# Kernel optimization log

Measured on AMD Instinct MI355X. Metric: run time of the kernel, lower is better.

Reference implementation:

```python
import jax, jax.numpy as jnp
import numpy as np

S, B, CIN, COUT, H, W, K = 4, 32, 128, 256, 16, 16, 3
D = CIN * K * K  # 1152, patch feature size = in_features
PRIOR_PREC = 1.0  # isotropic prior precision (prior_prec_full = PRIOR_PREC * I_D)
LOG_PREC_LR = 1.0


def _patches(x, k):
    # x: [N, C, H, W] -> [N, C*k*k, H, W]; channel-major patch ordering (matches torch unfold)
    pad = k // 2
    return jax.lax.conv_general_dilated_patches(
        x, (k, k), (1, 1), ((pad, pad), (pad, pad)),
        dimension_numbers=('NCHW', 'OIHW', 'NCHW'))


def setup_inputs() -> dict:
    key = jax.random.key(0)
    k1, k2, k3, k4 = jax.random.split(key, 4)
    X = jax.random.normal(k1, (S, B, CIN, H, W), jnp.float32)
    u = jax.random.normal(k2, (B, COUT, H, W), jnp.float32)
    log_prec_scaled = jax.random.normal(k3, (B,), jnp.float32)
    Z = jax.random.normal(k4, (S, COUT, D), jnp.float32)  # standard normal noise for rsample
    return {"X": X, "u": u, "log_prec_scaled": log_prec_scaled, "Z": Z}


def reference(X, u, log_prec_scaled, Z):
    Xi = X[:, :B]  # [S, B, CIN, H, W]
    sqrt_prec = jnp.exp(0.5 * LOG_PREC_LR * log_prec_scaled)[:, None, None, None]  # [B,1,1,1]
    Xil = sqrt_prec * Xi                     # [S, B, CIN, H, W]
    Yil = sqrt_prec * u                      # [B, COUT, H, W]

    # conv_mm: sufficient statistics via patch extraction
    P = _patches(Xil.reshape(S * B, CIN, H, W), K).reshape(S, B, D, H * W)
    Yf = Yil.reshape(B, COUT, H * W)
    XLX = jnp.einsum('sbdp,sbep->sde', P, P)       # [S, D, D]
    XLY = jnp.einsum('sbdp,bcp->sdc', P, Yf)       # [S, D, COUT]

    # rsample_logpq_weights
    prec = XLX + PRIOR_PREC * jnp.eye(D, dtype=XLX.dtype)   # [S, D, D]
    L = jnp.linalg.cholesky(prec)                            # [S, D, D], lower
    logdet_prec = 2.0 * jnp.sum(jnp.log(jnp.diagonal(L, axis1=-2, axis2=-1)), -1)  # [S]

    mu = jax.scipy.linalg.cho_solve((L, True), XLY)          # [S, D, COUT]
    # dW: solve L^T dW = Z (multi-RHS; L is shared across COUT)
    dW = jax.scipy.linalg.solve_triangular(L, jnp.swapaxes(Z, -1, -2), lower=True, trans='T')
    Wm = jnp.swapaxes(mu + dW, -1, -2)                       # [S, COUT, D]

    # logP: unnormalized MVN log-prob of each output neuron's weights under N(0, PRIOR_PREC^-1 I)
    logP = (0.5 * COUT * D * jnp.log(jnp.asarray(PRIOR_PREC, Wm.dtype))
            - 0.5 * PRIOR_PREC * jnp.sum(Wm * Wm, (-1, -2)))          # [S]
    logQ = -0.5 * jnp.sum(Z * Z, (-1, -2)) + 0.5 * COUT * logdet_prec  # [S]
    logpq = logP - logQ
    return Wm, logpq
```

## Files before the change

### kernel.cpp

```cpp
#include <hip/hip_runtime.h>
#include <math.h>

#define NS 4
#define NB 32
#define CIN 128
#define NCOUT 256
#define HWN 256
#define ND 1152
#define NK 8192
static const size_t D2 = (size_t)ND * ND;

typedef __attribute__((ext_vector_type(8))) short bf16x8;
typedef __attribute__((ext_vector_type(4))) float f32x4;

static __device__ inline unsigned short f2bf(float x) {
  unsigned int u = __float_as_uint(x);
  unsigned int r = (u + 0x7fffu + ((u >> 16) & 1u)) >> 16;
  return (unsigned short)r;
}
static __device__ inline float bf2f(unsigned short h) {
  return __uint_as_float(((unsigned int)h) << 16);
}
static __device__ inline float rdlane(float v, int l) {
  return __int_as_float(__builtin_amdgcn_readlane(__float_as_int(v), l));
}


__global__ void k_sqrtp(const float* __restrict__ lp, float* __restrict__ sp,
                        float* __restrict__ pp) {
  int b = threadIdx.x;
  if (b < NB) sp[b] = expf(0.5f * lp[b]);
  if (b < 8) pp[b] = 0.f;
}

__global__ __launch_bounds__(128) void k_patches(const float* __restrict__ X,
                                                 const float* __restrict__ sp,
                                                 unsigned short* __restrict__ Phi,
                                                 unsigned short* __restrict__ Plo) {
  int d = blockIdx.x, s = blockIdx.y, t = threadIdx.x;
  int c = d / 9, r = d % 9, ky = r / 3, kx = r % 3;
  int p0 = t * 2;
  int yy = (p0 >> 4) + ky - 1;
  int xx0 = (p0 & 15) + kx - 1;
  bool oky = (yy >= 0 && yy < 16);
  bool ok0 = oky && (xx0 >= 0) && (xx0 < 16);
  bool ok1 = oky && (xx0 + 1 >= 0) && (xx0 + 1 < 16);
  int xo = yy * 16 + xx0;
  size_t base = ((size_t)s * ND + d) * NK + p0;
  for (int b = 0; b < NB; ++b) {
    float sb = sp[b];
    const float* xb = X + ((size_t)(s * NB + b) * CIN + c) * HWN;
    float v0 = ok0 ? xb[xo] * sb : 0.f;
    float v1 = ok1 ? xb[xo + 1] * sb : 0.f;
    unsigned short h0 = f2bf(v0), h1 = f2bf(v1);
    unsigned short l0 = f2bf(v0 - bf2f(h0)), l1 = f2bf(v1 - bf2f(h1));
    size_t idx = base + (size_t)b * HWN;
    *(unsigned int*)(Phi + idx) = (unsigned int)h0 | ((unsigned int)h1 << 16);
    *(unsigned int*)(Plo + idx) = (unsigned int)l0 | ((unsigned int)l1 << 16);
  }
}

__global__ __launch_bounds__(128) void k_ytt(const float* __restrict__ u,
                                             const float* __restrict__ sp,
                                             unsigned short* __restrict__ Yhi,
                                             unsigned short* __restrict__ Ylo) {
  int c = blockIdx.x, t = threadIdx.x;
  int p0 = t * 2;
  for (int b = 0; b < NB; ++b) {
    float sb = sp[b];
    const float* ub = u + ((size_t)b * NCOUT + c) * HWN + p0;
    float v0 = ub[0] * sb, v1 = ub[1] * sb;
    unsigned short h0 = f2bf(v0), h1 = f2bf(v1);
    unsigned short l0 = f2bf(v0 - bf2f(h0)), l1 = f2bf(v1 - bf2f(h1));
    size_t idx = (size_t)c * NK + (size_t)b * HWN + p0;
    *(unsigned int*)(Yhi + idx) = (unsigned int)h0 | ((unsigned int)h1 << 16);
    *(unsigned int*)(Ylo + idx) = (unsigned int)l0 | ((unsigned int)l1 << 16);
  }
}

__global__ __launch_bounds__(256) void k_gemm_mfma(
    const unsigned short* __restrict__ Phi, const unsigned short* __restrict__ Plo,
    const unsigned short* __restrict__ Yhi, const unsigned short* __restrict__ Ylo,
    float* __restrict__ prec, float* __restrict__ prec2,
    float* __restrict__ XLY, float* __restrict__ XLY2) {
  int jt = blockIdx.x, it = blockIdx.y;
  int s = blockIdx.z >> 1, kp = blockIdx.z & 1;
  bool isX = (jt <= it);
  if (!isX && jt < 9) return;
  int i0 = it * 128;
  int j0;
  const unsigned short *Bh, *Bl;
  if (isX) {
    j0 = jt * 128;
    Bh = Phi + ((size_t)s * ND + j0) * NK;
    Bl = Plo + ((size_t)s * ND + j0) * NK;
  } else {
    j0 = (jt - 9) * 128;
    Bh = Yhi + (size_t)j0 * NK;
    Bl = Ylo + (size_t)j0 * NK;
  }
  const unsigned short* Ah = Phi + ((size_t)s * ND + i0) * NK;
  const unsigned short* Al = Plo + ((size_t)s * ND + i0) * NK;

  __shared__ unsigned short sAh[4096], sAl[4096], sBh[4096], sBl[4096];
  int tid = threadIdx.x, wave = tid >> 6, lane = tid & 63;
  int wr = wave >> 1, wc = wave & 1;

  f32x4 zero = {0.f, 0.f, 0.f, 0.f};
  f32x4 acc[4][4];
#pragma unroll
  for (int m = 0; m < 4; ++m)
#pragma unroll
    for (int n = 0; n < 4; ++n) acc[m][n] = zero;

  const unsigned short* srcs[4] = {Ah, Al, Bh, Bl};
  unsigned short* dsts[4] = {sAh, sAl, sBh, sBl};
  int r0l = lane >> 2;
  int ke = (lane & 3) * 8;
  int arow0 = wr * 64 + (lane & 15);
  int brow0 = wc * 64 + (lane & 15);
  int koff = (lane >> 4) * 8;

  int kbeg = kp * (NK / 2), kend = kbeg + NK / 2;
  for (int k0 = kbeg; k0 < kend; k0 += 32) {
    __syncthreads();
#pragma unroll
    for (int f = 0; f < 4; ++f) {
#pragma unroll
      for (int cc = 0; cc < 2; ++cc) {
        int c = wave * 2 + cc;
        const unsigned short* g = srcs[f] + (size_t)(c * 16 + r0l) * NK + k0 + ke;
        unsigned short* l = dsts[f] + c * 512;
        __builtin_amdgcn_global_load_lds(
            (const __attribute__((address_space(1))) void*)g,
            (__attribute__((address_space(3))) void*)l, 16, 0, 0);
      }
    }
    __syncthreads();
    bf16x8 ah[4], al[4], bh[4], bl[4];
#pragma unroll
    for (int m = 0; m < 4; ++m) {
      int off = (arow0 + m * 16) * 32 + koff;
      ah[m] = *(const bf16x8*)&sAh[off];
      al[m] = *(const bf16x8*)&sAl[off];
    }
#pragma unroll
    for (int n = 0; n < 4; ++n) {
      int off = (brow0 + n * 16) * 32 + koff;
      bh[n] = *(const bf16x8*)&sBh[off];
      bl[n] = *(const bf16x8*)&sBl[off];
    }
#pragma unroll
    for (int m = 0; m < 4; ++m)
#pragma unroll
      for (int n = 0; n < 4; ++n) {
        acc[m][n] = __builtin_amdgcn_mfma_f32_16x16x32_bf16(ah[m], bh[n], acc[m][n], 0, 0, 0);
        acc[m][n] = __builtin_amdgcn_mfma_f32_16x16x32_bf16(ah[m], bl[n], acc[m][n], 0, 0, 0);
        acc[m][n] = __builtin_amdgcn_mfma_f32_16x16x32_bf16(al[m], bh[n], acc[m][n], 0, 0, 0);
      }
  }

  if (isX) {
    float* base = (kp ? prec2 : prec) + (size_t)s * D2;
#pragma unroll
    for (int m = 0; m < 4; ++m) {
      int row = i0 + wr * 64 + m * 16 + (lane >> 4) * 4;
#pragma unroll
      for (int n = 0; n < 4; ++n) {
        int col = j0 + wc * 64 + n * 16 + (lane & 15);
        float* cp = base + (size_t)row * ND + col;
#pragma unroll
        for (int r = 0; r < 4; ++r) cp[(size_t)r * ND] = acc[m][n][r];
      }
    }
  } else {
    float* base = (kp ? XLY2 : XLY) + (size_t)s * ND * NCOUT;
#pragma unroll
    for (int m = 0; m < 4; ++m) {
      int row = i0 + wr * 64 + m * 16 + (lane >> 4) * 4;
#pragma unroll
      for (int n = 0; n < 4; ++n) {
        int col = j0 + wc * 64 + n * 16 + (lane & 15);
        float* cp = base + (size_t)row * NCOUT + col;
#pragma unroll
        for (int r = 0; r < 4; ++r) cp[(size_t)r * NCOUT] = acc[m][n][r];
      }
    }
  }
}

__global__ __launch_bounds__(256, 3) void k_chol_dag(
    float* __restrict__ L, const float* __restrict__ Lp2,
    float* __restrict__ iA64, float* __restrict__ logd,
    int* __restrict__ flags) {
  int t0 = blockIdx.x, s = blockIdx.y;
  int bi = 0;
  while ((bi + 1) * (bi + 2) / 2 <= t0) ++bi;
  int bj = t0 - bi * (bi + 1) / 2;
  int ib = bi * 64, jb = bj * 64;
  float* Ls = L + (size_t)s * D2;
  const float* Ps = Lp2 + (size_t)s * D2;
  int* fc = flags + s * 324;

  __shared__ float At[64][68];
  __shared__ float Bt[64][68];
  int tid = threadIdx.x, tx = tid & 15, ty = tid >> 4;
  int lane = tid & 63, w = tid >> 6;

  float acc[4][4];
#pragma unroll
  for (int r = 0; r < 4; ++r) {
    size_t idx = (size_t)(ib + ty * 4 + r) * ND + jb + tx * 4;
    float4 v = *(const float4*)(Ls + idx);
    float4 v2 = *(const float4*)(Ps + idx);
    acc[r][0] = v.x + v2.x; acc[r][1] = v.y + v2.y;
    acc[r][2] = v.z + v2.z; acc[r][3] = v.w + v2.w;
  }
  if (bi == bj) {
#pragma unroll
    for (int r = 0; r < 4; ++r)
#pragma unroll
      for (int e = 0; e < 4; ++e)
        if (ty * 4 + r == tx * 4 + e) acc[r][e] += 1.f;
  }

  for (int k = 0; k < bj; ++k) {
    if (tid == 0) {
      while (__hip_atomic_load(&fc[bi * 18 + k], __ATOMIC_RELAXED,
                               __HIP_MEMORY_SCOPE_AGENT) == 0)
        __builtin_amdgcn_s_sleep(2);
      while (__hip_atomic_load(&fc[bj * 18 + k], __ATOMIC_RELAXED,
                               __HIP_MEMORY_SCOPE_AGENT) == 0)
        __builtin_amdgcn_s_sleep(2);
      (void)__hip_atomic_load(&fc[bj * 18 + k], __ATOMIC_ACQUIRE,
                              __HIP_MEMORY_SCOPE_AGENT);
    }
    __syncthreads();
    int kb = k * 64;
    {
      int a2 = tid >> 2, km = (tid & 3) * 4;
#pragma unroll
      for (int m = 0; m < 4; ++m) {
        float4 v = *(const float4*)(Ls + (size_t)(ib + a2) * ND + kb + km + m * 16);
        At[km + m * 16 + 0][a2] = v.x;
        At[km + m * 16 + 1][a2] = v.y;
        At[km + m * 16 + 2][a2] = v.z;
        At[km + m * 16 + 3][a2] = v.w;
        float4 u4 = *(const float4*)(Ls + (size_t)(jb + a2) * ND + kb + km + m * 16);
        Bt[km + m * 16 + 0][a2] = u4.x;
        Bt[km + m * 16 + 1][a2] = u4.y;
        Bt[km + m * 16 + 2][a2] = u4.z;
        Bt[km + m * 16 + 3][a2] = u4.w;
      }
    }
    __syncthreads();
#pragma unroll
    for (int kc = 0; kc < 64; ++kc) {
      float4 a4 = *(const float4*)&At[kc][ty * 4];
      float4 b4 = *(const float4*)&Bt[kc][tx * 4];
      float ar[4] = {a4.x, a4.y, a4.z, a4.w};
      float br[4] = {b4.x, b4.y, b4.z, b4.w};
#pragma unroll
      for (int r = 0; r < 4; ++r)
#pragma unroll
        for (int e = 0; e < 4; ++e) acc[r][e] = fmaf(-ar[r], br[e], acc[r][e]);
    }
    __syncthreads();
  }

  if (bi == bj) {
#pragma unroll
    for (int r = 0; r < 4; ++r)
#pragma unroll
      for (int e = 0; e < 4; ++e) At[ty * 4 + r][tx * 4 + e] = acc[r][e];
    {
      int rr = tid >> 2, cb2 = (tid & 3) * 16;
#pragma unroll
      for (int m = 0; m < 16; ++m) Bt[rr][cb2 + m] = (rr == cb2 + m) ? 1.f : 0.f;
    }
    __syncthreads();
    float diagv = 1.f;
    for (int p = 0; p < 8; ++p) {
      int c0 = p * 8;
      if (w == 0) {
        float pa[8], xb[8];
#pragma unroll
        for (int e = 0; e < 8; ++e) {
          pa[e] = At[lane][c0 + e];
          xb[e] = Bt[c0 + e][lane];
        }
#pragma unroll
        for (int j = 0; j < 8; ++j) {
          float dj = rdlane(pa[j], c0 + j);
          float r0 = __builtin_amdgcn_rsqf(dj);
          r0 = r0 * (1.5f - 0.5f * dj * r0 * r0);
          pa[j] *= r0;
          float xj = xb[j] * r0;
          xb[j] = xj;
          if (lane == c0 + j) diagv = dj * r0;
#pragma unroll
          for (int e = j + 1; e < 8; ++e) {
            float sv = rdlane(pa[j], c0 + e);
            pa[e] = fmaf(-pa[j], sv, pa[e]);
            xb[e] = fmaf(-sv, xj, xb[e]);
          }
        }
#pragma unroll
        for (int e = 0; e < 8; ++e) {
          At[lane][c0 + e] = pa[e];
          Bt[c0 + e][lane] = xb[e];
        }
      }
      __syncthreads();
      if (p < 7) {
        float La[8], Xp[8];
#pragma unroll
        for (int e = 0; e < 8; ++e) {
          La[e] = At[lane][c0 + e];
          Xp[e] = Bt[c0 + e][lane];
        }
        for (int c = c0 + 8 + w; c < 64; c += 4) {
          float Lc[8];
#pragma unroll
          for (int e = 0; e < 8; ++e) Lc[e] = At[c][c0 + e];
          float v = At[lane][c], vb = Bt[c][lane];
#pragma unroll
          for (int e = 0; e < 8; ++e) {
            v = fmaf(-La[e], Lc[e], v);
            vb = fmaf(-Lc[e], Xp[e], vb);
          }
          At[lane][c] = v;
          Bt[c][lane] = vb;
        }
        __syncthreads();
      }
    }
    if (w == 0) logd[s * ND + ib + lane] = logf(diagv);
    {
      float* q = iA64 + (size_t)(s * 18 + bi) * 4096;
      int rr = tid >> 2, cb2 = (tid & 3) * 16;
#pragma unroll
      for (int m = 0; m < 4; ++m)
        *(float4*)(q + rr * 64 + cb2 + m * 4) = *(const float4*)&Bt[rr][cb2 + m * 4];
    }
    __threadfence();
    __syncthreads();
    if (tid == 0)
      __hip_atomic_store(&fc[bi * 18 + bi], 1, __ATOMIC_RELEASE,
                         __HIP_MEMORY_SCOPE_AGENT);
  } else {
#pragma unroll
    for (int r = 0; r < 4; ++r)
#pragma unroll
      for (int e = 0; e < 4; ++e) At[tx * 4 + e][ty * 4 + r] = acc[r][e];
    __syncthreads();
    if (tid == 0) {
      while (__hip_atomic_load(&fc[bj * 18 + bj], __ATOMIC_RELAXED,
                               __HIP_MEMORY_SCOPE_AGENT) == 0)
        __builtin_amdgcn_s_sleep(2);
      (void)__hip_atomic_load(&fc[bj * 18 + bj], __ATOMIC_ACQUIRE,
                              __HIP_MEMORY_SCOPE_AGENT);
    }
    __syncthreads();
    {
      const float* q = iA64 + (size_t)(s * 18 + bj) * 4096;
      int a2 = tid >> 2, km = (tid & 3) * 4;
#pragma unroll
      for (int m = 0; m < 4; ++m) {
        float4 v = *(const float4*)(q + a2 * 64 + km + m * 16);
        Bt[km + m * 16 + 0][a2] = v.x;
        Bt[km + m * 16 + 1][a2] = v.y;
        Bt[km + m * 16 + 2][a2] = v.z;
        Bt[km + m * 16 + 3][a2] = v.w;
      }
    }
    __syncthreads();
    float acc2[4][4] = {};
#pragma unroll
    for (int kc = 0; kc < 64; ++kc) {
      float4 a4 = *(const float4*)&At[kc][ty * 4];
      float4 b4 = *(const float4*)&Bt[kc][tx * 4];
      float ar[4] = {a4.x, a4.y, a4.z, a4.w};
      float br[4] = {b4.x, b4.y, b4.z, b4.w};
#pragma unroll
      for (int r = 0; r < 4; ++r)
#pragma unroll
        for (int e = 0; e < 4; ++e) acc2[r][e] = fmaf(ar[r], br[e], acc2[r][e]);
    }
#pragma unroll
    for (int r = 0; r < 4; ++r) {
      float4 v = {acc2[r][0], acc2[r][1], acc2[r][2], acc2[r][3]};
      *(float4*)(Ls + (size_t)(ib + ty * 4 + r) * ND + jb + tx * 4) = v;
    }
    __threadfence();
    __syncthreads();
    if (tid == 0)
      __hip_atomic_store(&fc[bi * 18 + bj], 1, __ATOMIC_RELEASE,
                         __HIP_MEMORY_SCOPE_AGENT);
  }
}

__global__ __launch_bounds__(256) void k_invd128(const float* __restrict__ L,
                                                 const float* __restrict__ iA64,
                                                 float* __restrict__ iD) {
  int q = blockIdx.x, s = blockIdx.y;
  int tid = threadIdx.x;
  const float* Ls = L + (size_t)s * D2;
  float* out = iD + ((size_t)(s * 9 + q)) * 16384;
  int b0 = q * 128;
  __shared__ float inv0[64][68];
  __shared__ float invCt[64][68];
  __shared__ float Bt[64][68];
  __shared__ float Tl[64][68];

  {
    const float* iA0 = iA64 + (size_t)(s * 18 + 2 * q) * 4096;
    const float* iA1 = iA0 + 4096;
    int i = tid >> 2, c4 = (tid & 3) * 16;
#pragma unroll
    for (int m = 0; m < 4; ++m) {
      float4 v0 = *(const float4*)(iA0 + i * 64 + c4 + m * 4);
      *(float4*)&inv0[i][c4 + m * 4] = v0;
      float4 v1 = *(const float4*)(iA1 + i * 64 + c4 + m * 4);
      invCt[c4 + m * 4 + 0][i] = v1.x;
      invCt[c4 + m * 4 + 1][i] = v1.y;
      invCt[c4 + m * 4 + 2][i] = v1.z;
      invCt[c4 + m * 4 + 3][i] = v1.w;
    }
    const float* src = Ls + (size_t)(b0 + 64 + i) * ND + b0 + c4;
#pragma unroll
    for (int m = 0; m < 4; ++m) {
      float4 v = *(const float4*)(src + m * 4);
      Bt[c4 + m * 4 + 0][i] = v.x;
      Bt[c4 + m * 4 + 1][i] = v.y;
      Bt[c4 + m * 4 + 2][i] = v.z;
      Bt[c4 + m * 4 + 3][i] = v.w;
    }
  }
  __syncthreads();

  int tx = tid & 15, ty = tid >> 4;
  float acc[4][4] = {};
#pragma unroll
  for (int k = 0; k < 64; ++k) {
    float a4[4], b4[4];
#pragma unroll
    for (int e = 0; e < 4; ++e) { a4[e] = Bt[k][ty * 4 + e]; b4[e] = inv0[k][tx * 4 + e]; }
#pragma unroll
    for (int r = 0; r < 4; ++r)
#pragma unroll
      for (int e = 0; e < 4; ++e) acc[r][e] = fmaf(a4[r], b4[e], acc[r][e]);
  }
#pragma unroll
  for (int r = 0; r < 4; ++r)
#pragma unroll
    for (int e = 0; e < 4; ++e) Tl[ty * 4 + r][tx * 4 + e] = acc[r][e];
  __syncthreads();
  float acc2[4][4] = {};
#pragma unroll
  for (int k = 0; k < 64; ++k) {
    float a4[4], b4[4];
#pragma unroll
    for (int e = 0; e < 4; ++e) { a4[e] = invCt[k][ty * 4 + e]; b4[e] = Tl[k][tx * 4 + e]; }
#pragma unroll
    for (int r = 0; r < 4; ++r)
#pragma unroll
      for (int e = 0; e < 4; ++e) acc2[r][e] = fmaf(a4[r], b4[e], acc2[r][e]);
  }
  {
    int rrow = tid >> 2, cc = (tid & 3) * 32;
    float* o = out + rrow * 128 + cc;
    if (cc < 64) {
#pragma unroll
      for (int m = 0; m < 8; ++m) {
        float4 v = {inv0[rrow][cc + m * 4 + 0], inv0[rrow][cc + m * 4 + 1],
                    inv0[rrow][cc + m * 4 + 2], inv0[rrow][cc + m * 4 + 3]};
        *(float4*)(o + m * 4) = v;
      }
    } else {
      float4 z = {0.f, 0.f, 0.f, 0.f};
#pragma unroll
      for (int m = 0; m < 8; ++m) *(float4*)(o + m * 4) = z;
    }
  }
#pragma unroll
  for (int r = 0; r < 4; ++r) {
    float4 v = {-acc2[r][0], -acc2[r][1], -acc2[r][2], -acc2[r][3]};
    *(float4*)(out + (size_t)(64 + ty * 4 + r) * 128 + tx * 4) = v;
  }
  {
    int i = tid >> 2, jc = (tid & 3) * 16;
#pragma unroll
    for (int m = 0; m < 4; ++m) {
      float4 v = {invCt[jc + m * 4 + 0][i], invCt[jc + m * 4 + 1][i],
                  invCt[jc + m * 4 + 2][i], invCt[jc + m * 4 + 3][i]};
      *(float4*)(out + (size_t)(64 + i) * 128 + 64 + jc + m * 4) = v;
    }
  }
}

__global__ __launch_bounds__(256) void k_solve2(
    const float* __restrict__ L, const float* __restrict__ iD,
    const float* __restrict__ B1, const float* __restrict__ B2,
    const float* __restrict__ Z, float* __restrict__ Xf, float* __restrict__ Xb,
    float* __restrict__ Wm, float* __restrict__ pp, int* __restrict__ flags) {
  int r = blockIdx.x, ct = blockIdx.y, s = blockIdx.z;
  int rb = r * 128, cb = ct * 64;
  const float* Ls = L + (size_t)s * D2;
  const float* Dq = iD + ((size_t)(s * 9 + r)) * 16384;
  float* Xfs = Xf + (size_t)s * ND * NCOUT;
  float* Xbs = Xb + (size_t)s * ND * NCOUT;
  int fbf = 1296 + (s * 4 + ct) * 9;
  int fbb = 1440 + (s * 4 + ct) * 9;

  __shared__ float sA[32][132];
  __shared__ float sB[32][68];
  __shared__ float red[8];
  int tid = threadIdx.x, tx = tid & 15, ty = tid >> 4;
  int wave = tid >> 6, lane = tid & 63;

  float acc[8][4];
#pragma unroll
  for (int ii = 0; ii < 8; ++ii) {
    size_t idx = (size_t)s * ND * NCOUT + (size_t)(rb + ty * 8 + ii) * NCOUT + cb + tx * 4;
    float4 v = *(const float4*)(B1 + idx);
    float4 v2 = *(const float4*)(B2 + idx);
    acc[ii][0] = v.x + v2.x; acc[ii][1] = v.y + v2.y;
    acc[ii][2] = v.z + v2.z; acc[ii][3] = v.w + v2.w;
  }
  for (int q = 0; q < r; ++q) {
    if (tid == 0) {
      while (__hip_atomic_load(&flags[fbf + q], __ATOMIC_RELAXED,
                               __HIP_MEMORY_SCOPE_AGENT) == 0)
        __builtin_amdgcn_s_sleep(2);
      (void)__hip_atomic_load(&flags[fbf + q], __ATOMIC_ACQUIRE,
                              __HIP_MEMORY_SCOPE_AGENT);
    }
    __syncthreads();
    int qb = q * 128;
    for (int kk = 0; kk < 4; ++kk) {
      __syncthreads();
      {
        int i = tid >> 1, kb = (tid & 1) * 16;
        const float* src = Ls + (size_t)(rb + i) * ND + qb + kk * 32 + kb;
#pragma unroll
        for (int m = 0; m < 4; ++m) {
          float4 v = *(const float4*)(src + m * 4);
          sA[kb + m * 4 + 0][i] = v.x;
          sA[kb + m * 4 + 1][i] = v.y;
          sA[kb + m * 4 + 2][i] = v.z;
          sA[kb + m * 4 + 3][i] = v.w;
        }
      }
      {
        int k = tid >> 3, jb2 = (tid & 7) * 8;
        const float* src = Xfs + (size_t)(qb + kk * 32 + k) * NCOUT + cb + jb2;
        float4 v0 = *(const float4*)src;
        float4 v1 = *(const float4*)(src + 4);
        *(float4*)&sB[k][jb2] = v0;
        *(float4*)&sB[k][jb2 + 4] = v1;
      }
      __syncthreads();
#pragma unroll
      for (int k = 0; k < 32; ++k) {
        float4 a0 = *(const float4*)&sA[k][ty * 8];
        float4 a1 = *(const float4*)&sA[k][ty * 8 + 4];
        float4 b0 = *(const float4*)&sB[k][tx * 4];
        float a[8] = {a0.x, a0.y, a0.z, a0.w, a1.x, a1.y, a1.z, a1.w};
        float b[4] = {b0.x, b0.y, b0.z, b0.w};
#pragma unroll
        for (int ii = 0; ii < 8; ++ii)
#pragma unroll
          for (int j = 0; j < 4; ++j) acc[ii][j] = fmaf(-a[ii], b[j], acc[ii][j]);
      }
    }
  }
  float acc2[8][4] = {};
  for (int kk = 0; kk < 4; ++kk) {
    __syncthreads();
    if ((ty >> 2) == kk) {
      int kloc = ty * 8 - kk * 32;
#pragma unroll
      for (int ii = 0; ii < 8; ++ii) {
        float4 v = {acc[ii][0], acc[ii][1], acc[ii][2], acc[ii][3]};
        *(float4*)&sB[kloc + ii][tx * 4] = v;
      }
    }
    {
      int i = tid >> 1, kb = (tid & 1) * 16;
      const float* src = Dq + (size_t)i * 128 + kk * 32 + kb;
#pragma unroll
      for (int m = 0; m < 4; ++m) {
        float4 v = *(const float4*)(src + m * 4);
        sA[kb + m * 4 + 0][i] = v.x;
        sA[kb + m * 4 + 1][i] = v.y;
        sA[kb + m * 4 + 2][i] = v.z;
        sA[kb + m * 4 + 3][i] = v.w;
      }
    }
    __syncthreads();
#pragma unroll
    for (int k = 0; k < 32; ++k) {
      float4 a0 = *(const float4*)&sA[k][ty * 8];
      float4 a1 = *(const float4*)&sA[k][ty * 8 + 4];
      float4 b0 = *(const float4*)&sB[k][tx * 4];
      float a[8] = {a0.x, a0.y, a0.z, a0.w, a1.x, a1.y, a1.z, a1.w};
      float b[4] = {b0.x, b0.y, b0.z, b0.w};
#pragma unroll
      for (int ii = 0; ii < 8; ++ii)
#pragma unroll
        for (int j = 0; j < 4; ++j) acc2[ii][j] = fmaf(a[ii], b[j], acc2[ii][j]);
    }
  }
#pragma unroll
  for (int ii = 0; ii < 8; ++ii) {
    float4 v = {acc2[ii][0], acc2[ii][1], acc2[ii][2], acc2[ii][3]};
    *(float4*)(Xfs + (size_t)(rb + ty * 8 + ii) * NCOUT + cb + tx * 4) = v;
  }
  __threadfence();
  __syncthreads();
  if (tid == 0)
    __hip_atomic_store(&flags[fbf + r], 1, __ATOMIC_RELEASE,
                       __HIP_MEMORY_SCOPE_AGENT);

#pragma unroll
  for (int ii = 0; ii < 8; ++ii)
#pragma unroll
    for (int j = 0; j < 4; ++j) acc[ii][j] = acc2[ii][j];

  float zp = 0.f;
  for (int kk = 0; kk < 4; ++kk) {
    __syncthreads();
    {
      int c = tid >> 2, d8 = (tid & 3) * 8;
      const float* src = Z + ((size_t)(s * NCOUT) + cb + c) * ND + rb + kk * 32 + d8;
      float4 v0 = *(const float4*)src;
      float4 v1 = *(const float4*)(src + 4);
      sA[d8 + 0][c] = v0.x; sA[d8 + 1][c] = v0.y; sA[d8 + 2][c] = v0.z; sA[d8 + 3][c] = v0.w;
      sA[d8 + 4][c] = v1.x; sA[d8 + 5][c] = v1.y; sA[d8 + 6][c] = v1.z; sA[d8 + 7][c] = v1.w;
      zp += v0.x * v0.x + v0.y * v0.y + v0.z * v0.z + v0.w * v0.w;
      zp += v1.x * v1.x + v1.y * v1.y + v1.z * v1.z + v1.w * v1.w;
    }
    __syncthreads();
    if ((ty >> 2) == kk) {
      int kloc = ty * 8 - kk * 32;
#pragma unroll
      for (int ii = 0; ii < 8; ++ii) {
        float4 v = *(const float4*)&sA[kloc + ii][tx * 4];
        acc[ii][0] += v.x; acc[ii][1] += v.y; acc[ii][2] += v.z; acc[ii][3] += v.w;
      }
    }
  }
#pragma unroll
  for (int m2 = 32; m2 >= 1; m2 >>= 1) zp += __shfl_xor(zp, m2, 64);
  if (lane == 0) red[wave] = zp;
  __syncthreads();
  if (tid == 0) atomicAdd(pp + s, red[0] + red[1] + red[2] + red[3]);

  for (int q = 8; q > r; --q) {
    if (tid == 0) {
      while (__hip_atomic_load(&flags[fbb + q], __ATOMIC_RELAXED,
                               __HIP_MEMORY_SCOPE_AGENT) == 0)
        __builtin_amdgcn_s_sleep(2);
      (void)__hip_atomic_load(&flags[fbb + q], __ATOMIC_ACQUIRE,
                              __HIP_MEMORY_SCOPE_AGENT);
    }
    __syncthreads();
    int qb = q * 128;
    for (int kk = 0; kk < 4; ++kk) {
      __syncthreads();
      {
        int k = tid >> 3, ib2 = (tid & 7) * 16;
        const float* src = Ls + (size_t)(qb + kk * 32 + k) * ND + rb + ib2;
#pragma unroll
        for (int m = 0; m < 4; ++m)
          *(float4*)&sA[k][ib2 + m * 4] = *(const float4*)(src + m * 4);
      }
      {
        int k = tid >> 3, jb2 = (tid & 7) * 8;
        const float* src = Xbs + (size_t)(qb + kk * 32 + k) * NCOUT + cb + jb2;
        float4 v0 = *(const float4*)src;
        float4 v1 = *(const float4*)(src + 4);
        *(float4*)&sB[k][jb2] = v0;
        *(float4*)&sB[k][jb2 + 4] = v1;
      }
      __syncthreads();
#pragma unroll
      for (int k = 0; k < 32; ++k) {
        float4 a0 = *(const float4*)&sA[k][ty * 8];
        float4 a1 = *(const float4*)&sA[k][ty * 8 + 4];
        float4 b0 = *(const float4*)&sB[k][tx * 4];
        float a[8] = {a0.x, a0.y, a0.z, a0.w, a1.x, a1.y, a1.z, a1.w};
        float b[4] = {b0.x, b0.y, b0.z, b0.w};
#pragma unroll
        for (int ii = 0; ii < 8; ++ii)
#pragma unroll
          for (int j = 0; j < 4; ++j) acc[ii][j] = fmaf(-a[ii], b[j], acc[ii][j]);
      }
    }
  }
#pragma unroll
  for (int ii = 0; ii < 8; ++ii)
#pragma unroll
    for (int j = 0; j < 4; ++j) acc2[ii][j] = 0.f;
  for (int kk = 0; kk < 4; ++kk) {
    __syncthreads();
    if ((ty >> 2) == kk) {
      int kloc = ty * 8 - kk * 32;
#pragma unroll
      for (int ii = 0; ii < 8; ++ii) {
        float4 v = {acc[ii][0], acc[ii][1], acc[ii][2], acc[ii][3]};
        *(float4*)&sB[kloc + ii][tx * 4] = v;
      }
    }
    {
      int k = tid >> 3, ib2 = (tid & 7) * 16;
      const float* src = Dq + (size_t)(kk * 32 + k) * 128 + ib2;
#pragma unroll
      for (int m = 0; m < 4; ++m)
        *(float4*)&sA[k][ib2 + m * 4] = *(const float4*)(src + m * 4);
    }
    __syncthreads();
#pragma unroll
    for (int k = 0; k < 32; ++k) {
      float4 a0 = *(const float4*)&sA[k][ty * 8];
      float4 a1 = *(const float4*)&sA[k][ty * 8 + 4];
      float4 b0 = *(const float4*)&sB[k][tx * 4];
      float a[8] = {a0.x, a0.y, a0.z, a0.w, a1.x, a1.y, a1.z, a1.w};
      float b[4] = {b0.x, b0.y, b0.z, b0.w};
#pragma unroll
      for (int ii = 0; ii < 8; ++ii)
#pragma unroll
        for (int j = 0; j < 4; ++j) acc2[ii][j] = fmaf(a[ii], b[j], acc2[ii][j]);
    }
  }
#pragma unroll
  for (int ii = 0; ii < 8; ++ii) {
    float4 v = {acc2[ii][0], acc2[ii][1], acc2[ii][2], acc2[ii][3]};
    *(float4*)(Xbs + (size_t)(rb + ty * 8 + ii) * NCOUT + cb + tx * 4) = v;
  }
  __threadfence();
  __syncthreads();
  if (tid == 0)
    __hip_atomic_store(&flags[fbb + r], 1, __ATOMIC_RELEASE,
                       __HIP_MEMORY_SCOPE_AGENT);
  float wp = 0.f;
#pragma unroll
  for (int ii = 0; ii < 8; ++ii)
#pragma unroll
    for (int j = 0; j < 4; ++j) wp += acc2[ii][j] * acc2[ii][j];
#pragma unroll
  for (int m2 = 32; m2 >= 1; m2 >>= 1) wp += __shfl_xor(wp, m2, 64);
  __syncthreads();
  if (lane == 0) red[wave] = wp;
  __syncthreads();
  if (tid == 0) atomicAdd(pp + 4 + s, red[0] + red[1] + red[2] + red[3]);
  for (int kk = 0; kk < 4; ++kk) {
    __syncthreads();
    if ((ty >> 2) == kk) {
      int kloc = ty * 8 - kk * 32;
#pragma unroll
      for (int ii = 0; ii < 8; ++ii) {
        float4 v = {acc2[ii][0], acc2[ii][1], acc2[ii][2], acc2[ii][3]};
        *(float4*)&sB[kloc + ii][tx * 4] = v;
      }
    }
    __syncthreads();
    {
      int c = tid >> 2, d8 = (tid & 3) * 8;
      float t0 = sB[d8 + 0][c], t1 = sB[d8 + 1][c], t2 = sB[d8 + 2][c], t3 = sB[d8 + 3][c];
      float t4 = sB[d8 + 4][c], t5 = sB[d8 + 5][c], t6 = sB[d8 + 6][c], t7 = sB[d8 + 7][c];
      float* dst = Wm + ((size_t)(s * NCOUT) + cb + c) * ND + rb + kk * 32 + d8;
      float4 w0 = {t0, t1, t2, t3}, w1 = {t4, t5, t6, t7};
      *(float4*)dst = w0;
      *(float4*)(dst + 4) = w1;
    }
  }
}

__global__ __launch_bounds__(256) void k_finalize(const float* __restrict__ logd,
                                                  const float* __restrict__ pp,
                                                  float* __restrict__ out) {
  int s = blockIdx.x, tid = threadIdx.x;
  __shared__ float r0[256];
  float l = 0.f;
  for (int i = tid; i < ND; i += 256) l += logd[s * ND + i];
  r0[tid] = l;
  __syncthreads();
  for (int off = 128; off; off >>= 1) {
    if (tid < off) r0[tid] += r0[tid + off];
    __syncthreads();
  }
  if (tid == 0) {
    float logdet = 2.0f * r0[0];
    out[s] = 0.5f * (pp[s] - pp[4 + s]) - 128.0f * logdet;
  }
}

extern "C" void kernel_launch(void* const* d_in, const int* in_sizes, int n_in,
                              void* d_out, int out_size, void* d_ws, size_t ws_size,
                              hipStream_t stream) {
  const float* X = (const float*)d_in[0];
  const float* u = (const float*)d_in[1];
  const float* lp = (const float*)d_in[2];
  const float* Z = (const float*)d_in[3];
  float* out = (float*)d_out;

  float* ws = (float*)d_ws;
  float* sp    = ws;
  float* invd  = sp + 64;
  float* logd  = invd + (size_t)NS * ND;
  float* pp    = logd + (size_t)NS * ND;
  int*   flags = (int*)(pp + 64);
  float* iD    = (float*)(flags + 2048);
  float* iA64  = iD + (size_t)NS * 9 * 16384;
  float* Xf    = iA64 + (size_t)NS * 18 * 4096;
  float* Xb    = Xf + (size_t)NS * ND * NCOUT;
  float* prec  = Xb + (size_t)NS * ND * NCOUT;
  float* prec2 = prec + (size_t)NS * D2;
  float* XLY   = prec2 + (size_t)NS * D2;
  float* XLY2  = XLY + (size_t)NS * ND * NCOUT;
  unsigned short* Phi = (unsigned short*)(XLY2 + (size_t)NS * ND * NCOUT);
  unsigned short* Plo = Phi + (size_t)NS * ND * NK;
  unsigned short* Yhi = Plo + (size_t)NS * ND * NK;
  unsigned short* Ylo = Yhi + (size_t)NCOUT * NK;

  hipMemsetAsync(flags, 0, 2048 * sizeof(int), stream);
  k_sqrtp<<<1, 64, 0, stream>>>(lp, sp, pp);
  k_patches<<<dim3(ND, NS), 128, 0, stream>>>(X, sp, Phi, Plo);
  k_ytt<<<NCOUT, 128, 0, stream>>>(u, sp, Yhi, Ylo);
  k_gemm_mfma<<<dim3(11, 9, NS * 2), 256, 0, stream>>>(Phi, Plo, Yhi, Ylo, prec,
                                                       prec2, XLY, XLY2);
  k_chol_dag<<<dim3(171, NS), 256, 0, stream>>>(prec, prec2, iA64, logd, flags);
  k_invd128<<<dim3(9, NS), 256, 0, stream>>>(prec, iA64, iD);
  k_solve2<<<dim3(9, 4, NS), 256, 0, stream>>>(prec, iD, XLY, XLY2, Z, Xf, Xb,
                                               out, pp, flags);
  k_finalize<<<NS, 256, 0, stream>>>(logd, pp, out + (size_t)NS * NCOUT * ND);
}
```

Before: 1.391 ms.

## Fuse diagonal-block Cholesky into last off-diagonal panel block; spin on flags in all threads

The factorization of each diagonal 64x64 block (except the first) moves into the block that computes the last sub-diagonal panel (bj == bi-1). That block applies the final rank-64 update itself and factors immediately, instead of a separate diagonal block waiting on flags. This removes one inter-block flag hop per step on the Cholesky critical path. A new set of flags (pd) signals when the partially updated diagonal tile has been written to global memory. Flag waits are now a helper in which every thread spins with a shorter sleep, replacing the tid==0 spin plus __syncthreads. This relies on the flags buffer being large enough and zeroed for the new pd region, and adds global traffic for the staged diagonal tile.

```diff
diff --git a/kernel.cpp b/kernel.cpp
--- a/kernel.cpp
+++ b/kernel.cpp
@@ -23,6 +23,11 @@
 }
 static __device__ inline float rdlane(float v, int l) {
   return __int_as_float(__builtin_amdgcn_readlane(__float_as_int(v), l));
+}
+static __device__ __forceinline__ void waitflag(const int* f) {
+  while (__hip_atomic_load(f, __ATOMIC_RELAXED, __HIP_MEMORY_SCOPE_AGENT) == 0)
+    __builtin_amdgcn_s_sleep(1);
+  (void)__hip_atomic_load(f, __ATOMIC_ACQUIRE, __HIP_MEMORY_SCOPE_AGENT);
 }
 
 
@@ -189,6 +194,92 @@
   }
 }
 
+
+static __device__ __forceinline__ void factor64(
+    float acc[4][4], float (&At)[64][68], float (&Bt)[64][68],
+    int tid, int lane, int w, int tx, int ty,
+    float* iA64q, float* logdq, int* flagq) {
+  __syncthreads();
+#pragma unroll
+  for (int r = 0; r < 4; ++r)
+#pragma unroll
+    for (int e = 0; e < 4; ++e) At[ty * 4 + r][tx * 4 + e] = acc[r][e];
+  {
+    int rr = tid >> 2, cb2 = (tid & 3) * 16;
+#pragma unroll
+    for (int m = 0; m < 16; ++m) Bt[rr][cb2 + m] = (rr == cb2 + m) ? 1.f : 0.f;
+  }
+  __syncthreads();
+  float diagv = 1.f;
+  for (int p = 0; p < 8; ++p) {
+    int c0 = p * 8;
+    if (w == 0) {
+      float pa[8], xb[8];
+#pragma unroll
+      for (int e = 0; e < 8; ++e) {
+        pa[e] = At[lane][c0 + e];
+        xb[e] = Bt[c0 + e][lane];
+      }
+#pragma unroll
+      for (int j = 0; j < 8; ++j) {
+        float dj = rdlane(pa[j], c0 + j);
+        float r0 = __builtin_amdgcn_rsqf(dj);
+        r0 = r0 * (1.5f - 0.5f * dj * r0 * r0);
+        pa[j] *= r0;
+        float xj = xb[j] * r0;
+        xb[j] = xj;
+        if (lane == c0 + j) diagv = dj * r0;
+#pragma unroll
+        for (int e = j + 1; e < 8; ++e) {
+          float sv = rdlane(pa[j], c0 + e);
+          pa[e] = fmaf(-pa[j], sv, pa[e]);
+          xb[e] = fmaf(-sv, xj, xb[e]);
+        }
+      }
+#pragma unroll
+      for (int e = 0; e < 8; ++e) {
+        At[lane][c0 + e] = pa[e];
+        Bt[c0 + e][lane] = xb[e];
+      }
+    }
+    __syncthreads();
+    if (p < 7) {
+      float La[8], Xp[8];
+#pragma unroll
+      for (int e = 0; e < 8; ++e) {
+        La[e] = At[lane][c0 + e];
+        Xp[e] = Bt[c0 + e][lane];
+      }
+      for (int c = c0 + 8 + w; c < 64; c += 4) {
+        float Lc[8];
+#pragma unroll
+        for (int e = 0; e < 8; ++e) Lc[e] = At[c][c0 + e];
+        float v = At[lane][c], vb = Bt[c][lane];
+#pragma unroll
+        for (int e = 0; e < 8; ++e) {
+          v = fmaf(-La[e], Lc[e], v);
+          vb = fmaf(-Lc[e], Xp[e], vb);
+        }
+        At[lane][c] = v;
+        Bt[c][lane] = vb;
+      }
+      __syncthreads();
+    }
+  }
+  if (w == 0) logdq[lane] = logf(diagv);
+  {
+    float* q = iA64q;
+    int rr = tid >> 2, cb2 = (tid & 3) * 16;
+#pragma unroll
+    for (int m = 0; m < 4; ++m)
+      *(float4*)(q + rr * 64 + cb2 + m * 4) = *(const float4*)&Bt[rr][cb2 + m * 4];
+  }
+  __threadfence();
+  __syncthreads();
+  if (tid == 0)
+    __hip_atomic_store(flagq, 1, __ATOMIC_RELEASE, __HIP_MEMORY_SCOPE_AGENT);
+}
+
 __global__ __launch_bounds__(256, 3) void k_chol_dag(
     float* __restrict__ L, const float* __restrict__ Lp2,
     float* __restrict__ iA64, float* __restrict__ logd,
@@ -201,6 +292,7 @@
   float* Ls = L + (size_t)s * D2;
   const float* Ps = Lp2 + (size_t)s * D2;
   int* fc = flags + s * 324;
+  int* pd = flags + 1584 + s * 18;
 
   __shared__ float At[64][68];
   __shared__ float Bt[64][68];
@@ -225,17 +317,8 @@
   }
 
   for (int k = 0; k < bj; ++k) {
-    if (tid == 0) {
-      while (__hip_atomic_load(&fc[bi * 18 + k], __ATOMIC_RELAXED,
-                               __HIP_MEMORY_SCOPE_AGENT) == 0)
-        __builtin_amdgcn_s_sleep(2);
-      while (__hip_atomic_load(&fc[bj * 18 + k], __ATOMIC_RELAXED,
-                               __HIP_MEMORY_SCOPE_AGENT) == 0)
-        __builtin_amdgcn_s_sleep(2);
-      (void)__hip_atomic_load(&fc[bj * 18 + k], __ATOMIC_ACQUIRE,
-                              __HIP_MEMORY_SCOPE_AGENT);
-    }
-    __syncthreads();
+    waitflag(&fc[bi * 18 + k]);
+    waitflag(&fc[bj * 18 + k]);
     int kb = k * 64;
     {
       int a2 = tid >> 2, km = (tid & 3) * 4;
@@ -269,99 +352,27 @@
   }
 
   if (bi == bj) {
+    if (bi == 0) {
+      factor64(acc, At, Bt, tid, lane, w, tx, ty,
+               iA64 + (size_t)(s * 18) * 4096, logd + (size_t)s * ND, &fc[0]);
+    } else {
+#pragma unroll
+      for (int r = 0; r < 4; ++r) {
+        float4 v = {acc[r][0], acc[r][1], acc[r][2], acc[r][3]};
+        *(float4*)(Ls + (size_t)(ib + ty * 4 + r) * ND + ib + tx * 4) = v;
+      }
+      __threadfence();
+      __syncthreads();
+      if (tid == 0)
+        __hip_atomic_store(&pd[bi], 1, __ATOMIC_RELEASE,
+                           __HIP_MEMORY_SCOPE_AGENT);
+    }
+  } else {
 #pragma unroll
     for (int r = 0; r < 4; ++r)
 #pragma unroll
-      for (int e = 0; e < 4; ++e) At[ty * 4 + r][tx * 4 + e] = acc[r][e];
-    {
-      int rr = tid >> 2, cb2 = (tid & 3) * 16;
-#pragma unroll
-      for (int m = 0; m < 16; ++m) Bt[rr][cb2 + m] = (rr == cb2 + m) ? 1.f : 0.f;
-    }
-    __syncthreads();
-    float diagv = 1.f;
-    for (int p = 0; p < 8; ++p) {
-      int c0 = p * 8;
-      if (w == 0) {
-        float pa[8], xb[8];
-#pragma unroll
-        for (int e = 0; e < 8; ++e) {
-          pa[e] = At[lane][c0 + e];
-          xb[e] = Bt[c0 + e][lane];
-        }
-#pragma unroll
-        for (int j = 0; j < 8; ++j) {
-          float dj = rdlane(pa[j], c0 + j);
-          float r0 = __builtin_amdgcn_rsqf(dj);
-          r0 = r0 * (1.5f - 0.5f * dj * r0 * r0);
-          pa[j] *= r0;
-          float xj = xb[j] * r0;
-          xb[j] = xj;
-          if (lane == c0 + j) diagv = dj * r0;
-#pragma unroll
-          for (int e = j + 1; e < 8; ++e) {
-            float sv = rdlane(pa[j], c0 + e);
-            pa[e] = fmaf(-pa[j], sv, pa[e]);
-            xb[e] = fmaf(-sv, xj, xb[e]);
-          }
-        }
-#pragma unroll
-        for (int e = 0; e < 8; ++e) {
-          At[lane][c0 + e] = pa[e];
-          Bt[c0 + e][lane] = xb[e];
-        }
-      }
-      __syncthreads();
-      if (p < 7) {
-        float La[8], Xp[8];
-#pragma unroll
-        for (int e = 0; e < 8; ++e) {
-          La[e] = At[lane][c0 + e];
-          Xp[e] = Bt[c0 + e][lane];
-        }
-        for (int c = c0 + 8 + w; c < 64; c += 4) {
-          float Lc[8];
-#pragma unroll
-          for (int e = 0; e < 8; ++e) Lc[e] = At[c][c0 + e];
-          float v = At[lane][c], vb = Bt[c][lane];
-#pragma unroll
-          for (int e = 0; e < 8; ++e) {
-            v = fmaf(-La[e], Lc[e], v);
-            vb = fmaf(-Lc[e], Xp[e], vb);
-          }
-          At[lane][c] = v;
-          Bt[c][lane] = vb;
-        }
-        __syncthreads();
-      }
-    }
-    if (w == 0) logd[s * ND + ib + lane] = logf(diagv);
-    {
-      float* q = iA64 + (size_t)(s * 18 + bi) * 4096;
-      int rr = tid >> 2, cb2 = (tid & 3) * 16;
-#pragma unroll
-      for (int m = 0; m < 4; ++m)
-        *(float4*)(q + rr * 64 + cb2 + m * 4) = *(const float4*)&Bt[rr][cb2 + m * 4];
-    }
-    __threadfence();
-    __syncthreads();
-    if (tid == 0)
-      __hip_atomic_store(&fc[bi * 18 + bi], 1, __ATOMIC_RELEASE,
-                         __HIP_MEMORY_SCOPE_AGENT);
-  } else {
-#pragma unroll
-    for (int r = 0; r < 4; ++r)
-#pragma unroll
       for (int e = 0; e < 4; ++e) At[tx * 4 + e][ty * 4 + r] = acc[r][e];
-    __syncthreads();
-    if (tid == 0) {
-      while (__hip_atomic_load(&fc[bj * 18 + bj], __ATOMIC_RELAXED,
-                               __HIP_MEMORY_SCOPE_AGENT) == 0)
-        __builtin_amdgcn_s_sleep(2);
-      (void)__hip_atomic_load(&fc[bj * 18 + bj], __ATOMIC_ACQUIRE,
-                              __HIP_MEMORY_SCOPE_AGENT);
-    }
-    __syncthreads();
+    waitflag(&fc[bj * 18 + bj]);
     {
       const float* q = iA64 + (size_t)(s * 18 + bj) * 4096;
       int a2 = tid >> 2, km = (tid & 3) * 4;
@@ -397,6 +408,34 @@
     if (tid == 0)
       __hip_atomic_store(&fc[bi * 18 + bj], 1, __ATOMIC_RELEASE,
                          __HIP_MEMORY_SCOPE_AGENT);
+
+    if (bj == bi - 1) {
+#pragma unroll
+      for (int r = 0; r < 4; ++r)
+#pragma unroll
+        for (int e = 0; e < 4; ++e) At[tx * 4 + e][ty * 4 + r] = acc2[r][e];
+      waitflag(&pd[bi]);
+#pragma unroll
+      for (int r = 0; r < 4; ++r) {
+        float4 v = *(const float4*)(Ls + (size_t)(ib + ty * 4 + r) * ND + ib + tx * 4);
+        acc[r][0] = v.x; acc[r][1] = v.y; acc[r][2] = v.z; acc[r][3] = v.w;
+      }
+      __syncthreads();
+#pragma unroll
+      for (int kc = 0; kc < 64; ++kc) {
+        float4 a4 = *(const float4*)&At[kc][ty * 4];
+        float4 b4 = *(const float4*)&At[kc][tx * 4];
+        float ar[4] = {a4.x, a4.y, a4.z, a4.w};
+        float br[4] = {b4.x, b4.y, b4.z, b4.w};
+#pragma unroll
+        for (int r = 0; r < 4; ++r)
+#pragma unroll
+          for (int e = 0; e < 4; ++e) acc[r][e] = fmaf(-ar[r], br[e], acc[r][e]);
+      }
+      factor64(acc, At, Bt, tid, lane, w, tx, ty,
+               iA64 + (size_t)(s * 18 + bi) * 4096, logd + (size_t)s * ND + ib,
+               &fc[bi * 18 + bi]);
+    }
   }
 }
 
@@ -529,14 +568,7 @@
     acc[ii][2] = v.z + v2.z; acc[ii][3] = v.w + v2.w;
   }
   for (int q = 0; q < r; ++q) {
-    if (tid == 0) {
-      while (__hip_atomic_load(&flags[fbf + q], __ATOMIC_RELAXED,
-                               __HIP_MEMORY_SCOPE_AGENT) == 0)
-        __builtin_amdgcn_s_sleep(2);
-      (void)__hip_atomic_load(&flags[fbf + q], __ATOMIC_ACQUIRE,
-                              __HIP_MEMORY_SCOPE_AGENT);
-    }
-    __syncthreads();
+    waitflag(&flags[fbf + q]);
     int qb = q * 128;
     for (int kk = 0; kk < 4; ++kk) {
       __syncthreads();
@@ -658,14 +690,7 @@
   if (tid == 0) atomicAdd(pp + s, red[0] + red[1] + red[2] + red[3]);
 
   for (int q = 8; q > r; --q) {
-    if (tid == 0) {
-      while (__hip_atomic_load(&flags[fbb + q], __ATOMIC_RELAXED,
-                               __HIP_MEMORY_SCOPE_AGENT) == 0)
-        __builtin_amdgcn_s_sleep(2);
-      (void)__hip_atomic_load(&flags[fbb + q], __ATOMIC_ACQUIRE,
-                              __HIP_MEMORY_SCOPE_AGENT);
-    }
-    __syncthreads();
+    waitflag(&flags[fbb + q]);
     int qb = q * 128;
     for (int kk = 0; kk < 4; ++kk) {
       __syncthreads();
```

Result: slower. 1.674 ms (+20.3%).
